# Kernel tuning notes

Hardware: AMD Instinct MI355X
Metric: run time of the kernel (lower is better)

Reference implementation:

```python
import jax, jax.numpy as jnp
import numpy as np

B, S, E, H = 2, 2048, 1024, 16
D = E // H  # head_dim = 64

def setup_inputs() -> dict:
    key = jax.random.key(0)
    ks = jax.random.split(key, 11)
    s = 1.0 / np.sqrt(E)
    inp = {
        'query': jax.random.normal(ks[0], (B, S, E), jnp.float32),
        'key':   jax.random.normal(ks[1], (B, S, E), jnp.float32),
        'value': jax.random.normal(ks[2], (B, S, E), jnp.float32),
        'Wq': jax.random.uniform(ks[3], (E, E), jnp.float32, -s, s),
        'bq': jax.random.uniform(ks[4], (E,), jnp.float32, -s, s),
        'Wk': jax.random.uniform(ks[5], (E, E), jnp.float32, -s, s),
        'bk': jax.random.uniform(ks[6], (E,), jnp.float32, -s, s),
        'Wv': jax.random.uniform(ks[7], (E, E), jnp.float32, -s, s),
        'bv': jax.random.uniform(ks[8], (E,), jnp.float32, -s, s),
        'Wo': jax.random.uniform(ks[9], (E, E), jnp.float32, -s, s),
        'bo': jax.random.uniform(ks[10], (E,), jnp.float32, -s, s),
    }
    return inp

def reference(query, key, value, Wq, bq, Wk, bk, Wv, bv, Wo, bo):
    # project and split heads: [B,S,E] -> [B,H,S,D]
    def proj(x, W, b):
        y = jnp.einsum('bse,fe->bsf', x, W) + b  # torch Linear: x @ W.T + b
        return y.reshape(B, S, H, D).transpose(0, 2, 1, 3)
    q = proj(query, Wq, bq)
    k = proj(key, Wk, bk)
    v = proj(value, Wv, bv)
    scores = jnp.einsum('bhqd,bhkd->bhqk', q, k) / jnp.sqrt(jnp.float32(D))
    attn = jax.nn.softmax(scores, axis=-1)
    out = jnp.einsum('bhqk,bhkd->bhqd', attn, v)  # [B,H,S,D]
    out = out.transpose(0, 2, 1, 3).reshape(B, S, E)
    return jnp.einsum('bse,fe->bsf', out, Wo) + bo
```

## Files before the change

### kernel.cpp

```cpp
#include <hip/hip_runtime.h>

#define B_ 2
#define S_ 2048
#define E_ 1024
#define H_ 16
#define D_ 64
#define M_ (B_*S_)
#define K_ E_

typedef __attribute__((ext_vector_type(8))) short  short8;
typedef __attribute__((ext_vector_type(4))) float  f32x4;
typedef __attribute__((ext_vector_type(8))) unsigned short u16x8;
typedef __attribute__((ext_vector_type(4))) unsigned short u16x4;
typedef __attribute__((ext_vector_type(4))) unsigned int   u32x4;

#define QSCALE 0.18033688011112042f

#if __has_builtin(__builtin_amdgcn_exp2f)
#define EXP2F(x) __builtin_amdgcn_exp2f(x)
#else
#define EXP2F(x) exp2f(x)
#endif

__device__ __forceinline__ unsigned short f2bf(float f) {
    unsigned u = __float_as_uint(f);
    u += 0x7fffu + ((u >> 16) & 1u);
    return (unsigned short)(u >> 16);
}

__device__ __forceinline__ unsigned cvtpk(float a, float b) {
    unsigned r;
    asm("v_cvt_pk_bf16_f32 %0, %1, %2" : "=v"(r) : "v"(a), "v"(b));
    return r;
}

__device__ __forceinline__ void gl_lds16(const ushort* g, ushort* l) {
    __builtin_amdgcn_global_load_lds((const __attribute__((address_space(1))) void*)g,
                                     (__attribute__((address_space(3))) void*)l,
                                     16, 0, 0);
}

#define FL_SYNC(N) do {                                                   \
    asm volatile("s_waitcnt vmcnt(" #N ")" ::: "memory");                 \
    __builtin_amdgcn_s_barrier();                                         \
    asm volatile("" ::: "memory");                                        \
} while (0)

#define WAITL0_BAR() do {                                                 \
    asm volatile("s_waitcnt lgkmcnt(0)" ::: "memory");                    \
    __builtin_amdgcn_s_barrier();                                         \
    asm volatile("" ::: "memory");                                        \
} while (0)

__global__ __launch_bounds__(256)
void cvt_all(const float* __restrict__ q, const float* __restrict__ k,
             const float* __restrict__ v, const float* __restrict__ wq,
             const float* __restrict__ wk, const float* __restrict__ wv,
             const float* __restrict__ wo, ushort* __restrict__ dst)
{
    const int bid = blockIdx.x;
    const float* src;
    size_t dof;
    int local;
    if (bid < 6144) {
        const int t = bid >> 11;
        src = (t == 0) ? q : (t == 1) ? k : v;
        dof = (size_t)t * 4194304u;
        local = bid & 2047;
    } else {
        const int r = bid - 6144;
        const int t = r >> 9;
        src = (t == 0) ? wq : (t == 1) ? wk : (t == 2) ? wv : wo;
        dof = 12582912u + (size_t)t * 1048576u;
        local = r & 511;
    }
    const size_t idx = (size_t)local * 2048 + threadIdx.x * 8;
    const float4 a = *(const float4*)(src + idx);
    const float4 b = *(const float4*)(src + idx + 4);
    u16x8 o;
    o[0] = f2bf(a.x); o[1] = f2bf(a.y); o[2] = f2bf(a.z); o[3] = f2bf(a.w);
    o[4] = f2bf(b.x); o[5] = f2bf(b.y); o[6] = f2bf(b.z); o[7] = f2bf(b.w);
    *(u16x8*)(dst + dof + idx) = o;
}

template<int SWAP>
__device__ __forceinline__ void qkv_core(const ushort* __restrict__ X,
                                         const ushort* __restrict__ W,
                                         int m0, int n0,
                                         f32x4 acc[8][4], ushort* sh)
{
    const int tid  = threadIdx.x;
    const int lane = tid & 63;
    const int w    = tid >> 6;
    const int wm   = w & 1;
    const int wn   = w >> 1;
    const int l15  = lane & 15, quad = lane >> 4;

    const int srow = lane >> 3, schunk = lane & 7;
    const int scol = (schunk ^ srow) * 8;
    const ushort* pa[4]; const ushort* pb[4]; int loff[4];
    #pragma unroll
    for (int i = 0; i < 4; ++i) {
        const int row = (w * 4 + i) * 8 + srow;
        pa[i] = X + (size_t)(m0 + row) * K_ + scol;
        pb[i] = W + (size_t)(n0 + row) * K_ + scol;
        loff[i] = (w * 4 + i) * 512 + lane * 8;
    }

    const f32x4 zero = {0.f, 0.f, 0.f, 0.f};
    #pragma unroll
    for (int mt = 0; mt < 8; ++mt)
        #pragma unroll
        for (int nt = 0; nt < 4; ++nt) acc[mt][nt] = zero;

    #pragma unroll
    for (int i = 0; i < 4; ++i) {
        gl_lds16(pa[i],      sh + loff[i]);
        gl_lds16(pb[i],      sh + 16384 + loff[i]);
    }
    #pragma unroll
    for (int i = 0; i < 4; ++i) {
        gl_lds16(pa[i] + 64, sh + 32768 + loff[i]);
        gl_lds16(pb[i] + 64, sh + 32768 + 16384 + loff[i]);
    }

    const int arow = wm * 128 + l15;
    const int brow = wn * 64 + l15;

    for (int t = 0; t < 16; ++t) {
        ushort* curA = sh + (t & 1) * 32768;
        ushort* curB = curA + 16384;

        if (t < 15) { FL_SYNC(8); } else { FL_SYNC(0); }

        __builtin_amdgcn_s_setprio(1);
        #pragma unroll
        for (int kc = 0; kc < 2; ++kc) {
            short8 bf[4];
            #pragma unroll
            for (int nt = 0; nt < 4; ++nt) {
                const int r = brow + nt * 16;
                bf[nt] = *(const short8*)(curB + r * 64 + (((kc * 4 + quad) ^ (r & 7)) * 8));
            }
            #pragma unroll
            for (int mt = 0; mt < 8; ++mt) {
                const int r = arow + mt * 16;
                const short8 af = *(const short8*)(curA + r * 64 + (((kc * 4 + quad) ^ (r & 7)) * 8));
                #pragma unroll
                for (int nt = 0; nt < 4; ++nt) {
                    if (SWAP)
                        acc[mt][nt] = __builtin_amdgcn_mfma_f32_16x16x32_bf16(bf[nt], af, acc[mt][nt], 0, 0, 0);
                    else
                        acc[mt][nt] = __builtin_amdgcn_mfma_f32_16x16x32_bf16(af, bf[nt], acc[mt][nt], 0, 0, 0);
                }
            }
        }
        __builtin_amdgcn_s_setprio(0);

        if (t + 2 < 16) {
            WAITL0_BAR();
            const int k0 = (t + 2) * 64;
            #pragma unroll
            for (int i = 0; i < 4; ++i) {
                gl_lds16(pa[i] + k0, curA + loff[i]);
                gl_lds16(pb[i] + k0, curB + loff[i]);
            }
        }
    }
}

__global__ __launch_bounds__(512, 2)
void gemm_qkv(const ushort* __restrict__ Xq, const ushort* __restrict__ Xk,
              const ushort* __restrict__ Xv, const ushort* __restrict__ Wq,
              const ushort* __restrict__ Wk, const ushort* __restrict__ Wv,
              const float* __restrict__ bq, const float* __restrict__ bk,
              const float* __restrict__ bv, ushort* __restrict__ Qh,
              ushort* __restrict__ Kh, ushort* __restrict__ Vt)
{
    __shared__ ushort sh[65536];
    const int z = blockIdx.z;
    const ushort* X = (z == 0) ? Xq : (z == 1) ? Xk : Xv;
    const ushort* W = (z == 0) ? Wq : (z == 1) ? Wk : Wv;
    const float* bias = (z == 0) ? bq : (z == 1) ? bk : bv;
    ushort* dst = (z == 0) ? Qh : (z == 1) ? Kh : Vt;

    const int m0 = blockIdx.y * 256, n0 = blockIdx.x * 256;
    f32x4 acc[8][4];
    const int lane = threadIdx.x & 63, w = threadIdx.x >> 6;
    const int wm = w & 1, wn = w >> 1;
    const int l15 = lane & 15, quad = lane >> 4;

    if (z < 2) {
        qkv_core<1>(X, W, m0, n0, acc, sh);
        const float qsc = (z == 0) ? QSCALE : 1.0f;
        #pragma unroll
        for (int nt = 0; nt < 4; ++nt) {
            const int nb = n0 + wn * 64 + nt * 16 + quad * 4;
            const int h = nb >> 6, d0 = nb & 63;
            const float4 b4 = *(const float4*)(bias + nb);
            const float bb4[4] = {b4.x, b4.y, b4.z, b4.w};
            #pragma unroll
            for (int mt = 0; mt < 8; ++mt) {
                const int tok = m0 + wm * 128 + mt * 16 + l15;
                const int b = tok >> 11, s = tok & (S_ - 1);
                u16x4 pk;
                #pragma unroll
                for (int r = 0; r < 4; ++r)
                    pk[r] = f2bf((acc[mt][nt][r] + bb4[r]) * qsc);
                *(u16x4*)&dst[(((size_t)(b * H_ + h) * S_) + s) * D_ + d0] = pk;
            }
        }
    } else {
        qkv_core<0>(X, W, m0, n0, acc, sh);
        float bias4[4];
        #pragma unroll
        for (int nt = 0; nt < 4; ++nt)
            bias4[nt] = bias[n0 + wn * 64 + nt * 16 + l15];
        #pragma unroll
        for (int mt = 0; mt < 8; ++mt) {
            const int mrow0 = m0 + wm * 128 + mt * 16 + (quad * 4);
            const int b = mrow0 >> 11;
            const int s0 = mrow0 & (S_ - 1);
            #pragma unroll
            for (int nt = 0; nt < 4; ++nt) {
                const int n = n0 + wn * 64 + nt * 16 + l15;
                const int h = n >> 6, d = n & 63;
                u16x4 pk;
                #pragma unroll
                for (int r = 0; r < 4; ++r) pk[r] = f2bf(acc[mt][nt][r] + bias4[nt]);
                *(u16x4*)&Vt[(((size_t)(b * H_ + h) * D_) + d) * S_ + s0] = pk;
            }
        }
    }
}

__global__ __launch_bounds__(256)
void gemm_out(const ushort* __restrict__ X, const ushort* __restrict__ W,
              const float* __restrict__ bias, float* __restrict__ out)
{
    __shared__ ushort Ast[128 * 32];
    __shared__ ushort Bst[64 * 32];
    const int m0 = blockIdx.y * 128, n0 = blockIdx.x * 64;
    const int tid = threadIdx.x, lane = tid & 63, w = tid >> 6;
    const int wm = w & 1, wn = w >> 1;
    const int l15 = lane & 15, quad = lane >> 4;
    const int r0 = tid >> 2, c8 = (tid & 3) * 8;
    const int kb = quad * 8;

    const f32x4 zero = {0.f, 0.f, 0.f, 0.f};
    f32x4 acc[4][2];
    #pragma unroll
    for (int mt = 0; mt < 4; ++mt)
        #pragma unroll
        for (int nt = 0; nt < 2; ++nt) acc[mt][nt] = zero;

    for (int k0 = 0; k0 < K_; k0 += 32) {
        __syncthreads();
        const ushort* ga = X + (size_t)(m0 + r0) * K_ + k0 + c8;
        gl_lds16(ga, Ast + tid * 8);
        gl_lds16(ga + (size_t)64 * K_, Ast + 2048 + tid * 8);
        const ushort* gb = W + (size_t)(n0 + r0) * K_ + k0 + c8;
        gl_lds16(gb, Bst + tid * 8);
        __syncthreads();

        short8 af[4], bf[2];
        #pragma unroll
        for (int mt = 0; mt < 4; ++mt)
            af[mt] = *(const short8*)(Ast + (wm * 64 + mt * 16 + l15) * 32 + kb);
        #pragma unroll
        for (int nt = 0; nt < 2; ++nt)
            bf[nt] = *(const short8*)(Bst + (wn * 32 + nt * 16 + l15) * 32 + kb);
        #pragma unroll
        for (int mt = 0; mt < 4; ++mt)
            #pragma unroll
            for (int nt = 0; nt < 2; ++nt)
                acc[mt][nt] = __builtin_amdgcn_mfma_f32_16x16x32_bf16(af[mt], bf[nt], acc[mt][nt], 0, 0, 0);
    }

    float bias2[2];
    #pragma unroll
    for (int nt = 0; nt < 2; ++nt)
        bias2[nt] = bias[n0 + wn * 32 + nt * 16 + l15];

    #pragma unroll
    for (int mt = 0; mt < 4; ++mt) {
        const int mrow0 = m0 + wm * 64 + mt * 16 + quad * 4;
        #pragma unroll
        for (int nt = 0; nt < 2; ++nt) {
            const int n = n0 + wn * 32 + nt * 16 + l15;
            #pragma unroll
            for (int r = 0; r < 4; ++r)
                out[(size_t)(mrow0 + r) * E_ + n] = acc[mt][nt][r] + bias2[nt];
        }
    }
}

#define NTILE (S_ / 64)
#define QBLK 128

__device__ __forceinline__ void flash_stage(const ushort* __restrict__ Kg,
                                            const ushort* __restrict__ Vg,
                                            size_t qk_off, size_t vt_off,
                                            ushort* sh, int j,
                                            int row0, int gcol0, int row1, int gcol1,
                                            int chunk0, int chunk1, int lane)
{
    ushort* sb = sh + 8192 + (j & 3) * 8192;
    const int j0n = j * 64;
    gl_lds16(Kg + qk_off + (size_t)(j0n + row0) * D_ + gcol0 * 8, sb + chunk0 * 512 + lane * 8);
    gl_lds16(Vg + vt_off + (size_t)row0 * S_ + j0n + gcol0 * 8, sb + 4096 + chunk0 * 512 + lane * 8);
    gl_lds16(Kg + qk_off + (size_t)(j0n + row1) * D_ + gcol1 * 8, sb + chunk1 * 512 + lane * 8);
    gl_lds16(Vg + vt_off + (size_t)row1 * S_ + j0n + gcol1 * 8, sb + 4096 + chunk1 * 512 + lane * 8);
}

__global__ __launch_bounds__(256, 2)
void flash_mfma(const ushort* __restrict__ Qg, const ushort* __restrict__ Kg,
                const ushort* __restrict__ Vg, ushort* __restrict__ AO)
{
    __shared__ ushort sh[40960];
    ushort* Qs = sh;

    const int tid = threadIdx.x, lane = tid & 63, w = tid >> 6;
    const int l15 = lane & 15, quad = lane >> 4;
    const int q0 = blockIdx.x * QBLK, h = blockIdx.y, b = blockIdx.z;
    const size_t qk_off = (size_t)(b * H_ + h) * S_ * D_;
    const size_t vt_off = (size_t)(b * H_ + h) * D_ * S_;

    const int chunk0 = w, chunk1 = w + 4;
    const int row0 = chunk0 * 8 + (lane >> 3);
    const int row1 = chunk1 * 8 + (lane >> 3);
    const int gcol0 = (lane & 7) ^ (row0 & 7);
    const int gcol1 = (lane & 7) ^ (row1 & 7);

    #pragma unroll
    for (int i = 0; i < 4; ++i) {
        const int qc = w + i * 4;
        const int qrow = qc * 8 + (lane >> 3);
        const int qg = (lane & 7) ^ (qrow & 7);
        gl_lds16(Qg + qk_off + (size_t)(q0 + qrow) * D_ + qg * 8,
                 Qs + qc * 512 + lane * 8);
    }
    flash_stage(Kg, Vg, qk_off, vt_off, sh, 0, row0, gcol0, row1, gcol1, chunk0, chunk1, lane);
    flash_stage(Kg, Vg, qk_off, vt_off, sh, 1, row0, gcol0, row1, gcol1, chunk0, chunk1, lane);

    FL_SYNC(8);

    f32x4 o[4][4];
    #pragma unroll
    for (int g = 0; g < 4; ++g)
        #pragma unroll
        for (int nt = 0; nt < 4; ++nt) o[g][nt] = {0.f, 0.f, 0.f, 0.f};
    float lsum[4] = {0.f, 0.f, 0.f, 0.f};

    const int qh  = (w >> 1) * 64;
    const int kvb = (w & 1) * 32;
    const int x7  = l15 & 7;
    const int rowA = (kvb + l15) * 64;
    const int rowB = (kvb + 16 + l15) * 64;
    const int gA = ((w & 1) * 4 + (quad >> 1)) ^ x7;
    const int gB = ((w & 1) * 4 + 2 + (quad >> 1)) ^ x7;
    const f32x4 zero = {0.f, 0.f, 0.f, 0.f};

    for (int j = 0; j < NTILE; ++j) {
        const ushort* Kb = sh + 8192 + (j & 3) * 8192;
        const ushort* Vb = Kb + 4096;
        if (j < NTILE - 1) { FL_SYNC(4); } else { FL_SYNC(0); }

        const short8 ka0 = *(const short8*)&Kb[rowA + ((quad ^ x7) * 8)];
        const short8 ka1 = *(const short8*)&Kb[rowA + (((4 + quad) ^ x7) * 8)];
        const short8 ka2 = *(const short8*)&Kb[rowB + ((quad ^ x7) * 8)];
        const short8 ka3 = *(const short8*)&Kb[rowB + (((4 + quad) ^ x7) * 8)];
        uint2 vvA[4], vvB[4];
        #pragma unroll
        for (int nt = 0; nt < 4; ++nt) {
            vvA[nt] = *(const uint2*)&Vb[(nt * 16 + l15) * 64 + gA * 8 + (quad & 1) * 4];
            vvB[nt] = *(const uint2*)&Vb[(nt * 16 + l15) * 64 + gB * 8 + (quad & 1) * 4];
        }

        if (j < NTILE - 2)
            flash_stage(Kg, Vg, qk_off, vt_off, sh, j + 2,
                        row0, gcol0, row1, gcol1, chunk0, chunk1, lane);

        __builtin_amdgcn_s_setprio(1);
        uint2 paLo[4], paHi[4];
        #pragma unroll
        for (int g = 0; g < 4; ++g) {
            const int qr = (qh + g * 16 + l15) * 64;
            const short8 qg0 = *(const short8*)&Qs[qr + ((quad ^ x7) * 8)];
            const short8 qg1 = *(const short8*)&Qs[qr + (((4 + quad) ^ x7) * 8)];
            f32x4 t = __builtin_amdgcn_mfma_f32_16x16x32_bf16(ka0, qg0, zero, 0, 0, 0);
            t = __builtin_amdgcn_mfma_f32_16x16x32_bf16(ka1, qg1, t, 0, 0, 0);
            f32x4 u = __builtin_amdgcn_mfma_f32_16x16x32_bf16(ka2, qg0, zero, 0, 0, 0);
            u = __builtin_amdgcn_mfma_f32_16x16x32_bf16(ka3, qg1, u, 0, 0, 0);
            {
                const float p0 = EXP2F(t[0]), p1 = EXP2F(t[1]);
                const float p2 = EXP2F(t[2]), p3 = EXP2F(t[3]);
                lsum[g] += (p0 + p1) + (p2 + p3);
                paLo[g].x = cvtpk(p0, p1);
                paLo[g].y = cvtpk(p2, p3);
            }
            {
                const float p0 = EXP2F(u[0]), p1 = EXP2F(u[1]);
                const float p2 = EXP2F(u[2]), p3 = EXP2F(u[3]);
                lsum[g] += (p0 + p1) + (p2 + p3);
                paHi[g].x = cvtpk(p0, p1);
                paHi[g].y = cvtpk(p2, p3);
            }
        }

        short8 pa8[4];
        #pragma unroll
        for (int g = 0; g < 4; ++g) {
            u32x4 pk;
            pk[0] = paLo[g].x; pk[1] = paLo[g].y;
            pk[2] = paHi[g].x; pk[3] = paHi[g].y;
            pa8[g] = __builtin_bit_cast(short8, pk);
        }
        #pragma unroll
        for (int nt = 0; nt < 4; ++nt) {
            u32x4 vk;
            vk[0] = vvA[nt].x; vk[1] = vvA[nt].y;
            vk[2] = vvB[nt].x; vk[3] = vvB[nt].y;
            const short8 vb8 = __builtin_bit_cast(short8, vk);
            #pragma unroll
            for (int g = 0; g < 4; ++g)
                o[g][nt] = __builtin_amdgcn_mfma_f32_16x16x32_bf16(pa8[g], vb8, o[g][nt], 0, 0, 0);
        }
        __builtin_amdgcn_s_setprio(0);
    }

    #pragma unroll
    for (int g = 0; g < 4; ++g) {
        lsum[g] += __shfl_xor(lsum[g], 16);
        lsum[g] += __shfl_xor(lsum[g], 32);
    }
    __syncthreads();
    float* fb = (float*)sh;
    if (w & 1) {
        #pragma unroll
        for (int g = 0; g < 4; ++g) {
            #pragma unroll
            for (int nt = 0; nt < 4; ++nt)
                #pragma unroll
                for (int r = 0; r < 4; ++r)
                    fb[(w >> 1) * 4096 + g * 1024 + (nt * 4 + r) * 64 + lane] = o[g][nt][r];
            if (quad == 0) fb[8192 + (w >> 1) * 64 + g * 16 + l15] = lsum[g];
        }
    }
    __syncthreads();
    if (!(w & 1)) {
        #pragma unroll
        for (int g = 0; g < 4; ++g) {
            #pragma unroll
            for (int nt = 0; nt < 4; ++nt)
                #pragma unroll
                for (int r = 0; r < 4; ++r)
                    o[g][nt][r] += fb[(w >> 1) * 4096 + g * 1024 + (nt * 4 + r) * 64 + lane];
            lsum[g] += fb[8192 + (w >> 1) * 64 + g * 16 + l15];
        }
        #pragma unroll
        for (int g = 0; g < 4; ++g) {
            const float inv = 1.0f / lsum[g];
            float invr[4];
            #pragma unroll
            for (int r = 0; r < 4; ++r)
                invr[r] = __shfl(inv, (lane & 0x30) | (quad * 4 + r));
            #pragma unroll
            for (int nt = 0; nt < 4; ++nt) {
                const int e = h * 64 + nt * 16 + l15;
                #pragma unroll
                for (int r = 0; r < 4; ++r) {
                    const int s = q0 + qh + g * 16 + quad * 4 + r;
                    AO[(size_t)(b * S_ + s) * E_ + e] = f2bf(o[g][nt][r] * invr[r]);
                }
            }
        }
    }
}

extern "C" void kernel_launch(void* const* d_in, const int* in_sizes, int n_in,
                              void* d_out, int out_size, void* d_ws, size_t ws_size,
                              hipStream_t stream) {
    const float* query = (const float*)d_in[0];
    const float* key   = (const float*)d_in[1];
    const float* value = (const float*)d_in[2];
    const float* Wq = (const float*)d_in[3];
    const float* bq = (const float*)d_in[4];
    const float* Wk = (const float*)d_in[5];
    const float* bk = (const float*)d_in[6];
    const float* Wv = (const float*)d_in[7];
    const float* bv = (const float*)d_in[8];
    const float* Wo = (const float*)d_in[9];
    const float* bo = (const float*)d_in[10];
    float* out = (float*)d_out;

    ushort* ws = (ushort*)d_ws;
    ushort* Xq  = ws;
    ushort* Xk  = ws + 4194304u;
    ushort* Xv  = ws + 8388608u;
    ushort* Wqb = ws + 12582912u;
    ushort* Wkb = ws + 13631488u;
    ushort* Wvb = ws + 14680064u;
    ushort* Wob = ws + 15728640u;
    ushort* Qh  = ws + 16777216u;
    ushort* Kh  = ws + 20971520u;
    ushort* Vt  = ws + 25165824u;
    ushort* AO  = ws + 29360128u;

    cvt_all<<<8192, 256, 0, stream>>>(query, key, value, Wq, Wk, Wv, Wo, ws);
    gemm_qkv<<<dim3(4, 16, 3), 512, 0, stream>>>(Xq, Xk, Xv, Wqb, Wkb, Wvb,
                                                 bq, bk, bv, Qh, Kh, Vt);
    flash_mfma<<<dim3(S_ / QBLK, H_, B_), 256, 0, stream>>>(Qh, Kh, Vt, AO);
    gemm_out<<<dim3(16, 32), 256, 0, stream>>>(AO, Wob, bo, out);
}
```

Measured before the change: 215.7 us.

## Multi-buffer LDS prefetch pipeline in output projection GEMM

Replaces the single-buffered load/sync/compute loop in the output projection GEMM with a 4-slot LDS ring buffer. Loads run two K-tiles ahead, and a FL_SYNC wait-count replaces the double __syncthreads, so global-to-LDS traffic overlaps the MFMA work. MFMA issue is also wrapped in s_setprio raises. This grows shared memory per block, which may reduce occupancy, and relies on the existing FL_SYNC macro being correct for ordering.

```diff
diff --git a/kernel.cpp b/kernel.cpp
--- a/kernel.cpp
+++ b/kernel.cpp
@@ -238,8 +238,7 @@
 void gemm_out(const ushort* __restrict__ X, const ushort* __restrict__ W,
               const float* __restrict__ bias, float* __restrict__ out)
 {
-    __shared__ ushort Ast[128 * 32];
-    __shared__ ushort Bst[64 * 32];
+    __shared__ ushort sh[24576];
     const int m0 = blockIdx.y * 128, n0 = blockIdx.x * 64;
     const int tid = threadIdx.x, lane = tid & 63, w = tid >> 6;
     const int wm = w & 1, wn = w >> 1;
@@ -247,6 +246,9 @@
     const int r0 = tid >> 2, c8 = (tid & 3) * 8;
     const int kb = quad * 8;
 
+    const ushort* ga = X + (size_t)(m0 + r0) * K_ + c8;
+    const ushort* gb = W + (size_t)(n0 + r0) * K_ + c8;
+
     const f32x4 zero = {0.f, 0.f, 0.f, 0.f};
     f32x4 acc[4][2];
     #pragma unroll
@@ -254,27 +256,42 @@
         #pragma unroll
         for (int nt = 0; nt < 2; ++nt) acc[mt][nt] = zero;
 
-    for (int k0 = 0; k0 < K_; k0 += 32) {
-        __syncthreads();
-        const ushort* ga = X + (size_t)(m0 + r0) * K_ + k0 + c8;
-        gl_lds16(ga, Ast + tid * 8);
-        gl_lds16(ga + (size_t)64 * K_, Ast + 2048 + tid * 8);
-        const ushort* gb = W + (size_t)(n0 + r0) * K_ + k0 + c8;
-        gl_lds16(gb, Bst + tid * 8);
-        __syncthreads();
+    #pragma unroll
+    for (int t0 = 0; t0 < 2; ++t0) {
+        ushort* sb = sh + t0 * 6144;
+        gl_lds16(ga + t0 * 32,                 sb + tid * 8);
+        gl_lds16(ga + t0 * 32 + (size_t)64 * K_, sb + 2048 + tid * 8);
+        gl_lds16(gb + t0 * 32,                 sb + 4096 + tid * 8);
+    }
+
+    for (int t = 0; t < 32; ++t) {
+        ushort* sb = sh + (t & 3) * 6144;
+
+        if (t < 31) { FL_SYNC(3); } else { FL_SYNC(0); }
 
         short8 af[4], bf[2];
         #pragma unroll
         for (int mt = 0; mt < 4; ++mt)
-            af[mt] = *(const short8*)(Ast + (wm * 64 + mt * 16 + l15) * 32 + kb);
+            af[mt] = *(const short8*)(sb + (wm * 64 + mt * 16 + l15) * 32 + kb);
         #pragma unroll
         for (int nt = 0; nt < 2; ++nt)
-            bf[nt] = *(const short8*)(Bst + (wn * 32 + nt * 16 + l15) * 32 + kb);
+            bf[nt] = *(const short8*)(sb + 4096 + (wn * 32 + nt * 16 + l15) * 32 + kb);
+
+        if (t + 2 < 32) {
+            ushort* nb = sh + ((t + 2) & 3) * 6144;
+            const int k0 = (t + 2) * 32;
+            gl_lds16(ga + k0,                 nb + tid * 8);
+            gl_lds16(ga + k0 + (size_t)64 * K_, nb + 2048 + tid * 8);
+            gl_lds16(gb + k0,                 nb + 4096 + tid * 8);
+        }
+
+        __builtin_amdgcn_s_setprio(1);
         #pragma unroll
         for (int mt = 0; mt < 4; ++mt)
             #pragma unroll
             for (int nt = 0; nt < 2; ++nt)
                 acc[mt][nt] = __builtin_amdgcn_mfma_f32_16x16x32_bf16(af[mt], bf[nt], acc[mt][nt], 0, 0, 0);
+        __builtin_amdgcn_s_setprio(0);
     }
 
     float bias2[2];
```

Measured after the change: 210.0 us. -2.6%, faster.
